# Kernel optimization log

Hardware: AMD Instinct MI355X
Metric: run time of the kernel (lower is better)

## Reference

```python
import jax, jax.numpy as jnp
import numpy as np
import math

M = 8                      # multiplicity (channels per irrep)
COMBOS = [(0,0,0),(0,1,1),(1,0,1),(1,1,0),(1,1,1),(2,1,1)]  # (edge_l, node_l, out_l)

def _cg_coeff(j1, m1, j2, m2, j3, m3):
    # standard (Racah) complex Clebsch-Gordan coefficient <j1 m1 j2 m2 | j3 m3>
    if m3 != m1 + m2:
        return 0.0
    f = math.factorial
    vmin = max(0, j2 - j3 - m1, j1 + m2 - j3)
    vmax = min(j1 + j2 - j3, j1 - m1, j2 + m2)
    pref = (2*j3 + 1) * f(j3+j1-j2) * f(j3-j1+j2) * f(j1+j2-j3) / f(j1+j2+j3+1)
    pref *= f(j3+m3) * f(j3-m3) * f(j1-m1) * f(j1+m1) * f(j2-m2) * f(j2+m2)
    s = 0.0
    for v in range(vmin, vmax + 1):
        s += (-1)**v / (f(v) * f(j1+j2-j3-v) * f(j1-m1-v) * f(j2+m2-v)
                        * f(j3-j2+m1+v) * f(j3-j1-m2+v))
    return math.sqrt(pref) * s

def _su2_cg(l1, l2, l3):
    C = np.zeros((2*l1+1, 2*l2+1, 2*l3+1), dtype=np.complex128)
    for m1 in range(-l1, l1+1):
        for m2 in range(-l2, l2+1):
            m3 = m1 + m2
            if -l3 <= m3 <= l3:
                C[m1+l1, m2+l2, m3+l3] = _cg_coeff(l1, m1, l2, m2, l3, m3)
    return C

def _qmat(l):
    # real -> complex spherical-harmonic change of basis (e3nn convention)
    q = np.zeros((2*l+1, 2*l+1), dtype=np.complex128)
    for m in range(-l, 0):
        q[l+m, l+abs(m)] = 1/np.sqrt(2)
        q[l+m, l-abs(m)] = -1j/np.sqrt(2)
    q[l, l] = 1.0
    for m in range(1, l+1):
        q[l+m, l+abs(m)] = (-1)**m / np.sqrt(2)
        q[l+m, l-abs(m)] = 1j * (-1)**m / np.sqrt(2)
    return (-1j)**l * q

def _so3_cg(l1, l2, l3):
    # real-basis CG, normalized to unit Frobenius norm (matches e3nn _so3_clebsch_gordan)
    C = np.einsum('ij,kl,mn,ikn->jlm', _qmat(l1), _qmat(l2),
                  np.conj(_qmat(l3)).T, _su2_cg(l1, l2, l3))
    assert np.abs(C.imag).max() < 1e-6
    C = C.real
    return C / np.linalg.norm(C)

CG = {c: jnp.asarray(_so3_cg(*c), dtype=jnp.float32) for c in COMBOS}


def setup_inputs() -> dict:
    N, E = 100000, 1600000
    ks = jax.random.split(jax.random.key(0), 6)
    return {
        'node_irreps': jax.random.normal(ks[0], (N, 4*M), jnp.float32),
        'edge_index': jax.random.randint(ks[1], (2, E), 0, N, dtype=jnp.int32),
        'sh0': jax.random.normal(ks[2], (E, 1), jnp.float32),
        'sh1': jax.random.normal(ks[3], (E, 3), jnp.float32),
        'sh2': jax.random.normal(ks[4], (E, 5), jnp.float32),
        'W': jax.random.normal(ks[5], (len(COMBOS), M, M), jnp.float32),
    }


def reference(node_irreps, edge_index, sh0, sh1, sh2, W):
    N, E = node_irreps.shape[0], edge_index.shape[1]
    src = node_irreps[edge_index[0]]                    # gather: [E, 4M]
    feats = {0: src[:, :M][:, :, None],                 # scalar channels [E, M, 1]
             1: src[:, M:].reshape(E, M, 3)}            # vector channels [E, M, 3]
    sh = {0: sh0, 1: sh1, 2: sh2}
    msg = {0: jnp.zeros((E, M, 1), node_irreps.dtype),
           1: jnp.zeros((E, M, 3), node_irreps.dtype)}
    for idx, (le, ln, lo) in enumerate(COMBOS):
        # per-edge CG tensor product: [de,dn,do] x [E,de] x [E,M,dn] -> [E,M,do]
        base = jnp.einsum('ijk,ei,emj->emk', CG[(le, ln, lo)], sh[le], feats[ln])
        # channel-mixing scalar weights (in_channel -> out_channel)
        msg[lo] = msg[lo] + jnp.einsum('io,eik->eok', W[idx], base)
    tgt = edge_index[1]
    agg0 = jax.ops.segment_sum(msg[0].reshape(E, M), tgt, num_segments=N)     # [N, M]
    agg1 = jax.ops.segment_sum(msg[1].reshape(E, 3*M), tgt, num_segments=N)   # [N, 3M]
    return jnp.concatenate([agg0, agg1], axis=1)
```

## Files before the change

### kernel.cpp

```cpp
#include <hip/hip_runtime.h>

#define THREADS 256


__global__ __launch_bounds__(THREADS) void k_hist(const int* __restrict__ tgt,
                                                  int* __restrict__ cnt, int E) {
    int e = blockIdx.x * THREADS + threadIdx.x;
    if (e < E) atomicAdd(&cnt[tgt[e]], 1);
}

__global__ __launch_bounds__(THREADS) void k_scan_partial(const int* __restrict__ cnt,
                                                          int* __restrict__ bsum, int N) {
    __shared__ int lds[THREADS];
    int base = blockIdx.x * 1024 + threadIdx.x * 4;
    int s = 0;
    #pragma unroll
    for (int k = 0; k < 4; ++k) { int i = base + k; if (i < N) s += cnt[i]; }
    lds[threadIdx.x] = s; __syncthreads();
    for (int off = THREADS / 2; off > 0; off >>= 1) {
        if (threadIdx.x < off) lds[threadIdx.x] += lds[threadIdx.x + off];
        __syncthreads();
    }
    if (threadIdx.x == 0) bsum[blockIdx.x] = lds[0];
}

__global__ __launch_bounds__(1024) void k_scan_bsum(int* __restrict__ bsum, int NB) {
    __shared__ int lds[1024];
    int t = threadIdx.x;
    int v = (t < NB) ? bsum[t] : 0;
    lds[t] = v; __syncthreads();
    for (int off = 1; off < 1024; off <<= 1) {
        int x = (t >= off) ? lds[t - off] : 0;
        __syncthreads();
        lds[t] += x;
        __syncthreads();
    }
    if (t < NB) bsum[t] = lds[t] - v;
}

__global__ __launch_bounds__(THREADS) void k_scan_final(const int* __restrict__ cnt,
                                                        const int* __restrict__ bsum,
                                                        int* __restrict__ rowptr,
                                                        int* __restrict__ cursor,
                                                        int N, int E) {
    __shared__ int lds[THREADS];
    int base = blockIdx.x * 1024 + threadIdx.x * 4;
    int v[4]; int local = 0;
    #pragma unroll
    for (int k = 0; k < 4; ++k) {
        int i = base + k;
        v[k] = (i < N) ? cnt[i] : 0;
        local += v[k];
    }
    lds[threadIdx.x] = local; __syncthreads();
    for (int off = 1; off < THREADS; off <<= 1) {
        int x = (threadIdx.x >= off) ? lds[threadIdx.x - off] : 0;
        __syncthreads();
        lds[threadIdx.x] += x;
        __syncthreads();
    }
    int p = lds[threadIdx.x] - local + bsum[blockIdx.x];
    #pragma unroll
    for (int k = 0; k < 4; ++k) {
        int i = base + k;
        if (i < N) { rowptr[i] = p; cursor[i] = p; p += v[k]; }
    }
    if (blockIdx.x == 0 && threadIdx.x == 0) rowptr[N] = E;
}


__global__ __launch_bounds__(THREADS) void k_scatter(const int* __restrict__ eidx,
                                                     int* __restrict__ cursor,
                                                     const float* __restrict__ sh0,
                                                     const float* __restrict__ sh1,
                                                     const float* __restrict__ sh2,
                                                     float* __restrict__ payload,
                                                     int E) {
    int e = blockIdx.x * THREADS + threadIdx.x;
    if (e >= E) return;
    int src = eidx[e];
    int tgt = eidx[E + e];

    float4 p0 = make_float4(sh0[e], sh1[3*e+0], sh1[3*e+1], sh1[3*e+2]);
    float4 p1 = make_float4(sh2[5*e+0], sh2[5*e+1], sh2[5*e+2], sh2[5*e+3]);
    float2 p2 = make_float2(sh2[5*e+4], __int_as_float(src));

    int pos = atomicAdd(&cursor[tgt], 1);

    float* pr = payload + (size_t)pos * 16;
    *(float4*)(pr + 0) = p0;
    *(float4*)(pr + 4) = p1;
    *(float2*)(pr + 8) = p2;
}


#define ACC_STRIDE 15

__global__ __launch_bounds__(THREADS) void k_agg2(const float* __restrict__ node,
                                                  const int*   __restrict__ rowptr,
                                                  const float* __restrict__ payload,
                                                  const float* __restrict__ W,
                                                  float*       __restrict__ out, int N) {
    __shared__ float sW[384];
    __shared__ float sAcc[32 * 8 * ACC_STRIDE];
    for (int t = threadIdx.x; t < 384; t += THREADS) sW[t] = W[t];
    __syncthreads();

    constexpr float IS3  = 0.57735026918962576f;
    constexpr float IS6  = 0.40824829046386302f;
    constexpr float IS10 = 0.31622776601683794f;
    constexpr float IS30 = 0.18257418583505536f;

    const int nodeSlot = threadIdx.x >> 3;
    const int i        = threadIdx.x & 7;
    const int n        = blockIdx.x * 32 + nodeSlot;

    float a[14];
    #pragma unroll
    for (int k = 0; k < 14; ++k) a[k] = 0.f;

    if (n < N) {
        const int jbeg = rowptr[n];
        const int jend = rowptr[n + 1];

        if (jbeg < jend) {
            const float* pr = payload + (size_t)jbeg * 16;
            float4 c0 = *(const float4*)(pr + 0);
            float4 c1 = *(const float4*)(pr + 4);
            float2 c2 = *(const float2*)(pr + 8);

            for (int j = jbeg; j < jend; ++j) {
                float4 n0, n1; float2 n2;
                if (j + 1 < jend) {
                    const float* prn = payload + (size_t)(j + 1) * 16;
                    n0 = *(const float4*)(prn + 0);
                    n1 = *(const float4*)(prn + 4);
                    n2 = *(const float2*)(prn + 8);
                }

                const int src = __float_as_int(c2.y);
                const float* nr = node + (size_t)src * 32;
                const float f0 = nr[i];
                const float x  = nr[8 + 3*i + 0];
                const float y  = nr[8 + 3*i + 1];
                const float z  = nr[8 + 3*i + 2];

                const float s  = c0.x, u0 = c0.y, u1 = c0.z, u2 = c0.w;
                const float q0 = c1.x, q1 = c1.y, q2 = c1.z, q3 = c1.w, q4 = c2.x;

                const float Q00 = -q2*IS30 - q4*IS10;
                const float Q01 =  q1*IS10;
                const float Q02 =  q0*IS10;
                const float Q11 =  2.0f*q2*IS30;
                const float Q12 =  q3*IS10;
                const float Q22 = -q2*IS30 + q4*IS10;

                a[0]  += s * f0;
                a[1]  += u0*x + u1*y + u2*z;
                a[2]  += s * x;
                a[3]  += s * y;
                a[4]  += s * z;
                a[5]  += f0 * u0;
                a[6]  += f0 * u1;
                a[7]  += f0 * u2;
                a[8]  += u1*z - u2*y;
                a[9]  += u2*x - u0*z;
                a[10] += u0*y - u1*x;
                a[11] += Q00*x + Q01*y + Q02*z;
                a[12] += Q01*x + Q11*y + Q12*z;
                a[13] += Q02*x + Q12*y + Q22*z;

                c0 = n0; c1 = n1; c2 = n2;
            }
        }
    }

    #pragma unroll
    for (int k = 1; k < 8; ++k) a[k] *= IS3;
    #pragma unroll
    for (int k = 8; k < 11; ++k) a[k] *= IS6;

    float* myAcc = &sAcc[(nodeSlot * 8 + i) * ACC_STRIDE];
    #pragma unroll
    for (int k = 0; k < 14; ++k) myAcc[k] = a[k];
    __syncthreads();

    if (n < N) {
        const int o = i;
        float o0 = 0.f, ox = 0.f, oy = 0.f, oz = 0.f;
        #pragma unroll
        for (int ii = 0; ii < 8; ++ii) {
            const float* A = &sAcc[(nodeSlot * 8 + ii) * ACC_STRIDE];
            const float w0 = sW[  0 + ii*8 + o];
            const float w1 = sW[ 64 + ii*8 + o];
            const float w2 = sW[128 + ii*8 + o];
            const float w3 = sW[192 + ii*8 + o];
            const float w4 = sW[256 + ii*8 + o];
            const float w5 = sW[320 + ii*8 + o];
            o0 += w0*A[0]  + w3*A[1];
            ox += w1*A[2]  + w2*A[5] + w4*A[8]  + w5*A[11];
            oy += w1*A[3]  + w2*A[6] + w4*A[9]  + w5*A[12];
            oz += w1*A[4]  + w2*A[7] + w4*A[10] + w5*A[13];
        }
        float* orow = out + (size_t)n * 32;
        orow[o]         = o0;
        orow[8 + 3*o+0] = ox;
        orow[8 + 3*o+1] = oy;
        orow[8 + 3*o+2] = oz;
    }
}


__global__ __launch_bounds__(THREADS) void msg_kernel_atomic(
    const float* __restrict__ node,
    const int*   __restrict__ eidx,
    const float* __restrict__ sh0,
    const float* __restrict__ sh1,
    const float* __restrict__ sh2,
    const float* __restrict__ W,
    float*       __restrict__ out,
    int E)
{
    __shared__ float sW[384];
    for (int t = threadIdx.x; t < 384; t += THREADS) sW[t] = W[t];
    __syncthreads();

    int e = blockIdx.x * THREADS + threadIdx.x;
    if (e >= E) return;

    constexpr float IS3  = 0.57735026918962576f;
    constexpr float IS6  = 0.40824829046386302f;
    constexpr float IS10 = 0.31622776601683794f;
    constexpr float IS30 = 0.18257418583505536f;

    const int src = eidx[e];
    const int tgt = eidx[E + e];

    const float s  = sh0[e];
    const float u0 = sh1[3*e+0], u1 = sh1[3*e+1], u2 = sh1[3*e+2];
    const float q0 = sh2[5*e+0], q1 = sh2[5*e+1], q2 = sh2[5*e+2],
                q3 = sh2[5*e+3], q4 = sh2[5*e+4];

    const float Q00 = -q2*IS30 - q4*IS10;
    const float Q01 =  q1*IS10;
    const float Q02 =  q0*IS10;
    const float Q11 =  2.0f*q2*IS30;
    const float Q12 =  q3*IS10;
    const float Q22 = -q2*IS30 + q4*IS10;

    float f[32];
    {
        const float4* nr = (const float4*)(node + (size_t)src * 32);
        #pragma unroll
        for (int i = 0; i < 8; ++i) {
            float4 v = nr[i];
            f[4*i+0]=v.x; f[4*i+1]=v.y; f[4*i+2]=v.z; f[4*i+3]=v.w;
        }
    }

    float msg[32];
    #pragma unroll
    for (int j = 0; j < 32; ++j) msg[j] = 0.0f;

    const float s13 = s * IS3;

    #pragma unroll
    for (int i = 0; i < 8; ++i) {
        const float f0i = f[i];
        const float x = f[8+3*i+0], y = f[8+3*i+1], z = f[8+3*i+2];
        const float c0  = s * f0i;
        const float c3  = IS3 * (u0*x + u1*y + u2*z);
        const float p2  = IS3 * f0i;
        const float c1x = s13*x, c1y = s13*y, c1z = s13*z;
        const float c2x = p2*u0, c2y = p2*u1, c2z = p2*u2;
        const float c4x = IS6*(u1*z - u2*y);
        const float c4y = IS6*(u2*x - u0*z);
        const float c4z = IS6*(u0*y - u1*x);
        const float c5x = Q00*x + Q01*y + Q02*z;
        const float c5y = Q01*x + Q11*y + Q12*z;
        const float c5z = Q02*x + Q12*y + Q22*z;

        float wr[6][8];
        #pragma unroll
        for (int c = 0; c < 6; ++c) {
            float4 aa = *(const float4*)&sW[c*64 + i*8 + 0];
            float4 bb = *(const float4*)&sW[c*64 + i*8 + 4];
            wr[c][0]=aa.x; wr[c][1]=aa.y; wr[c][2]=aa.z; wr[c][3]=aa.w;
            wr[c][4]=bb.x; wr[c][5]=bb.y; wr[c][6]=bb.z; wr[c][7]=bb.w;
        }

        #pragma unroll
        for (int o = 0; o < 8; ++o) {
            msg[o] += wr[0][o]*c0 + wr[3][o]*c3;
            msg[8+3*o+0] += wr[1][o]*c1x + wr[2][o]*c2x + wr[4][o]*c4x + wr[5][o]*c5x;
            msg[8+3*o+1] += wr[1][o]*c1y + wr[2][o]*c2y + wr[4][o]*c4y + wr[5][o]*c5y;
            msg[8+3*o+2] += wr[1][o]*c1z + wr[2][o]*c2z + wr[4][o]*c4z + wr[5][o]*c5z;
        }
    }

    float* orow = out + (size_t)tgt * 32;
    #pragma unroll
    for (int j = 0; j < 32; ++j) unsafeAtomicAdd(orow + j, msg[j]);
}


extern "C" void kernel_launch(void* const* d_in, const int* in_sizes, int n_in,
                              void* d_out, int out_size, void* d_ws, size_t ws_size,
                              hipStream_t stream) {
    const float* node = (const float*)d_in[0];
    const int*   eidx = (const int*)d_in[1];
    const float* sh0  = (const float*)d_in[2];
    const float* sh1  = (const float*)d_in[3];
    const float* sh2  = (const float*)d_in[4];
    const float* W    = (const float*)d_in[5];
    float* out = (float*)d_out;

    const int E = in_sizes[2];
    const int N = in_sizes[0] / 32;
    const int NB = (N + 1023) / 1024;

    size_t int_words = (size_t)(N + 1) + N + N + 1024;
    size_t pay_off_w = (int_words + 15) & ~(size_t)15;
    size_t need      = (pay_off_w + (size_t)E * 16) * sizeof(float);

    if (ws_size >= need && NB <= 1024) {
        int* rowptr = (int*)d_ws;
        int* cursor = rowptr + (N + 1);
        int* cnt    = cursor + N;
        int* bsum   = cnt + N;
        float* payload = (float*)d_ws + pay_off_w;

        hipMemsetAsync(cnt, 0, (size_t)N * sizeof(int), stream);

        k_hist<<<(E + THREADS - 1) / THREADS, THREADS, 0, stream>>>(eidx + E, cnt, E);
        k_scan_partial<<<NB, THREADS, 0, stream>>>(cnt, bsum, N);
        k_scan_bsum<<<1, 1024, 0, stream>>>(bsum, NB);
        k_scan_final<<<NB, THREADS, 0, stream>>>(cnt, bsum, rowptr, cursor, N, E);
        k_scatter<<<(E + THREADS - 1) / THREADS, THREADS, 0, stream>>>(
            eidx, cursor, sh0, sh1, sh2, payload, E);

        k_agg2<<<(N + 31) / 32, THREADS, 0, stream>>>(node, rowptr, payload, W, out, N);
    } else {
        hipMemsetAsync(d_out, 0, (size_t)out_size * sizeof(float), stream);
        msg_kernel_atomic<<<(E + THREADS - 1) / THREADS, THREADS, 0, stream>>>(
            node, eidx, sh0, sh1, sh2, W, out, E);
    }
}
```

Before: 351.0 us.

## Pack edge payload in original order and aggregate via permutation index

The scatter kernel now writes each edge's packed payload contiguously at its original edge index, making those stores coalesced, and records a CSR permutation array through the atomic cursor instead. The aggregation kernel reads perm[j] and then gathers the payload indirectly. This trades scattered 40-byte writes for scattered 4-byte writes, but adds an extra dependent load and turns the aggregation's sequential payload reads into random reads. It also writes 64 bytes per edge instead of 40.

Result: slower. 400.6 us (+14.2%).

```diff
diff --git a/kernel.cpp b/kernel.cpp
--- a/kernel.cpp
+++ b/kernel.cpp
@@ -69,13 +69,14 @@
 }
 
 
-__global__ __launch_bounds__(THREADS) void k_scatter(const int* __restrict__ eidx,
-                                                     int* __restrict__ cursor,
-                                                     const float* __restrict__ sh0,
-                                                     const float* __restrict__ sh1,
-                                                     const float* __restrict__ sh2,
-                                                     float* __restrict__ payload,
-                                                     int E) {
+__global__ __launch_bounds__(THREADS) void k_pack_perm(const int* __restrict__ eidx,
+                                                       int* __restrict__ cursor,
+                                                       const float* __restrict__ sh0,
+                                                       const float* __restrict__ sh1,
+                                                       const float* __restrict__ sh2,
+                                                       float* __restrict__ payload,
+                                                       int* __restrict__ perm,
+                                                       int E) {
     int e = blockIdx.x * THREADS + threadIdx.x;
     if (e >= E) return;
     int src = eidx[e];
@@ -83,21 +84,22 @@
 
     float4 p0 = make_float4(sh0[e], sh1[3*e+0], sh1[3*e+1], sh1[3*e+2]);
     float4 p1 = make_float4(sh2[5*e+0], sh2[5*e+1], sh2[5*e+2], sh2[5*e+3]);
-    float2 p2 = make_float2(sh2[5*e+4], __int_as_float(src));
+    float4 p2 = make_float4(sh2[5*e+4], __int_as_float(src), 0.f, 0.f);
+    float4 p3 = make_float4(0.f, 0.f, 0.f, 0.f);
+
+    float4* pr = (float4*)(payload + (size_t)e * 16);
+    pr[0] = p0; pr[1] = p1; pr[2] = p2; pr[3] = p3;
 
     int pos = atomicAdd(&cursor[tgt], 1);
-
-    float* pr = payload + (size_t)pos * 16;
-    *(float4*)(pr + 0) = p0;
-    *(float4*)(pr + 4) = p1;
-    *(float2*)(pr + 8) = p2;
+    perm[pos] = e;
 }
 
 
 #define ACC_STRIDE 15
 
-__global__ __launch_bounds__(THREADS) void k_agg2(const float* __restrict__ node,
+__global__ __launch_bounds__(THREADS) void k_agg3(const float* __restrict__ node,
                                                   const int*   __restrict__ rowptr,
+                                                  const int*   __restrict__ perm,
                                                   const float* __restrict__ payload,
                                                   const float* __restrict__ W,
                                                   float*       __restrict__ out, int N) {
@@ -124,7 +126,8 @@
         const int jend = rowptr[n + 1];
 
         if (jbeg < jend) {
-            const float* pr = payload + (size_t)jbeg * 16;
+            int ecur = perm[jbeg];
+            const float* pr = payload + (size_t)ecur * 16;
             float4 c0 = *(const float4*)(pr + 0);
             float4 c1 = *(const float4*)(pr + 4);
             float2 c2 = *(const float2*)(pr + 8);
@@ -132,7 +135,8 @@
             for (int j = jbeg; j < jend; ++j) {
                 float4 n0, n1; float2 n2;
                 if (j + 1 < jend) {
-                    const float* prn = payload + (size_t)(j + 1) * 16;
+                    int enxt = perm[j + 1];
+                    const float* prn = payload + (size_t)enxt * 16;
                     n0 = *(const float4*)(prn + 0);
                     n1 = *(const float4*)(prn + 4);
                     n2 = *(const float2*)(prn + 8);
@@ -319,7 +323,7 @@
     const int N = in_sizes[0] / 32;
     const int NB = (N + 1023) / 1024;
 
-    size_t int_words = (size_t)(N + 1) + N + N + 1024;
+    size_t int_words = (size_t)(N + 1) + N + N + 1024 + (size_t)E;
     size_t pay_off_w = (int_words + 15) & ~(size_t)15;
     size_t need      = (pay_off_w + (size_t)E * 16) * sizeof(float);
 
@@ -328,6 +332,7 @@
         int* cursor = rowptr + (N + 1);
         int* cnt    = cursor + N;
         int* bsum   = cnt + N;
+        int* perm   = bsum + 1024;
         float* payload = (float*)d_ws + pay_off_w;
 
         hipMemsetAsync(cnt, 0, (size_t)N * sizeof(int), stream);
@@ -336,10 +341,10 @@
         k_scan_partial<<<NB, THREADS, 0, stream>>>(cnt, bsum, N);
         k_scan_bsum<<<1, 1024, 0, stream>>>(bsum, NB);
         k_scan_final<<<NB, THREADS, 0, stream>>>(cnt, bsum, rowptr, cursor, N, E);
-        k_scatter<<<(E + THREADS - 1) / THREADS, THREADS, 0, stream>>>(
-            eidx, cursor, sh0, sh1, sh2, payload, E);
-
-        k_agg2<<<(N + 31) / 32, THREADS, 0, stream>>>(node, rowptr, payload, W, out, N);
+        k_pack_perm<<<(E + THREADS - 1) / THREADS, THREADS, 0, stream>>>(
+            eidx, cursor, sh0, sh1, sh2, payload, perm, E);
+
+        k_agg3<<<(N + 31) / 32, THREADS, 0, stream>>>(node, rowptr, perm, payload, W, out, N);
     } else {
         hipMemsetAsync(d_out, 0, (size_t)out_size * sizeof(float), stream);
         msg_kernel_atomic<<<(E + THREADS - 1) / THREADS, THREADS, 0, stream>>>(
```
